# Performance work log

Measured on AMD Instinct MI355X. Metric: run time of the kernel, lower is better.

## Reference

```python
import jax, jax.numpy as jnp
import numpy as np

E = 8        # moe_num_experts
TOPK = 2     # moe_topk
H = 1024     # hidden_size
I = 1024     # intermediate_size
ISH = I * 2  # shared experts intermediate (intermediate_size * moe_num_shared_experts)
B, S = 2, 1024


def setup_inputs() -> dict:
    key = jax.random.key(0)
    ks = jax.random.split(key, 7)
    s = 0.02
    return {
        "hidden_states": jax.random.normal(ks[0], (B, S, H), jnp.float32),
        "w_router": jax.random.normal(ks[1], (H, E), jnp.float32) * s,
        "fc1_w": jax.random.normal(ks[2], (E, H, 2 * I), jnp.float32) * s,
        "fc2_w": jax.random.normal(ks[3], (E, I, H), jnp.float32) * s,
        "gate_w": jax.random.normal(ks[4], (H, ISH), jnp.float32) * s,
        "up_w": jax.random.normal(ks[5], (H, ISH), jnp.float32) * s,
        "down_w": jax.random.normal(ks[6], (ISH, H), jnp.float32) * s,
    }


def reference(hidden_states, w_router, fc1_w, fc2_w, gate_w, up_w, down_w):
    orig_shape = hidden_states.shape
    x = hidden_states.reshape(-1, orig_shape[-1])  # [N, H]

    # --- router: top-k + softmax over the top-k logits ---
    logits = x @ w_router                               # [N, E]
    top_logits, top_idx = jax.lax.top_k(logits, TOPK)   # [N, K]
    scores = jax.nn.softmax(top_logits, axis=-1)        # [N, K]

    # --- permute tokens so same-expert tokens are contiguous ---
    flat_idx = top_idx.reshape(-1)                      # [N*K]
    sorted_idx = jnp.argsort(flat_idx)                  # [N*K]
    permuted = x[sorted_idx // TOPK]                    # [N*K, H]
    eid = flat_idx[sorted_idx]                          # expert id per permuted slot

    # --- grouped expert SwiGLU MLP (masked per-expert GEMMs; masked rows
    #     contribute exactly zero since silu(0)*0 = 0 and 0 @ W = 0) ---
    out_perm = jnp.zeros((permuted.shape[0], orig_shape[-1]), x.dtype)
    for e in range(E):
        m = (eid == e).astype(x.dtype)[:, None]         # [N*K, 1]
        h1 = (permuted * m) @ fc1_w[e]                  # [N*K, 2I]
        proj, gate = jnp.split(h1, 2, axis=-1)
        out_perm = out_perm + (jax.nn.silu(proj) * gate) @ fc2_w[e]

    # --- unpermute and combine with router scores ---
    unperm = jnp.zeros_like(out_perm).at[sorted_idx].set(out_perm)  # [N*K, H]
    moe_out = (unperm.reshape(-1, TOPK, orig_shape[-1]) * scores[:, :, None]).sum(axis=1)
    moe_out = moe_out.reshape(orig_shape)

    # --- shared experts (LlamaMLP, SwiGLU) ---
    shared = (jax.nn.silu(hidden_states @ gate_w) * (hidden_states @ up_w)) @ down_w
    return moe_out + shared
```

## Files before the change

kernel.cpp:

```cpp
#include <hip/hip_runtime.h>
#include <cstdint>


#define E_ 8
#define H_ 1024
#define I_ 1024
#define ISH_ 2048
#define NTOK 2048

typedef unsigned short u16;
using bf16x8 = __attribute__((ext_vector_type(8))) __bf16;
using f32x4  = __attribute__((ext_vector_type(4))) float;

__device__ __forceinline__ u16 f2bf(float f) {
  union { float f; unsigned u; } v; v.f = f;
  unsigned r = v.u + 0x7fffu + ((v.u >> 16) & 1u);
  return (u16)(r >> 16);
}
__device__ __forceinline__ float bf2f(u16 u) {
  union { unsigned u; float f; } v; v.u = ((unsigned)u) << 16; return v.f;
}

typedef __attribute__((address_space(1))) const void glb_v;
typedef __attribute__((address_space(3))) void lds_v;
__device__ __forceinline__ void gl16(const void* g, void* l) {
  __builtin_amdgcn_global_load_lds((glb_v*)g, (lds_v*)l, 16, 0, 0);
}

__device__ __forceinline__ void router_body(const float* __restrict__ x,
                                            const float* __restrict__ wr,
                                            float* __restrict__ scores,
                                            int* __restrict__ cnt,
                                            int* __restrict__ list, int tk) {
  int lane = threadIdx.x & 63;
  const float* xr = x + (size_t)tk * H_;
  float acc[E_];
#pragma unroll
  for (int e = 0; e < E_; ++e) acc[e] = 0.f;
  int h0 = lane * 16;
#pragma unroll 4
  for (int i = 0; i < 16; ++i) {
    float xv = xr[h0 + i];
    const float* w = wr + (size_t)(h0 + i) * E_;
#pragma unroll
    for (int e = 0; e < E_; ++e) acc[e] = fmaf(xv, w[e], acc[e]);
  }
#pragma unroll
  for (int off = 32; off > 0; off >>= 1) {
#pragma unroll
    for (int e = 0; e < E_; ++e) acc[e] += __shfl_xor(acc[e], off, 64);
  }
  if (lane == 0) {
    int e0 = 0; float m0 = acc[0];
#pragma unroll
    for (int e = 1; e < E_; ++e) if (acc[e] > m0) { m0 = acc[e]; e0 = e; }
    int e1 = -1; float m1 = -1e30f;
#pragma unroll
    for (int e = 0; e < E_; ++e) if (e != e0 && acc[e] > m1) { m1 = acc[e]; e1 = e; }
    float s0 = 1.f / (1.f + __expf(m1 - m0));
    scores[tk * 2 + 0] = s0;
    scores[tk * 2 + 1] = 1.f - s0;
    int p0 = atomicAdd(&cnt[e0], 1); list[e0 * NTOK + p0] = tk * 2;
    int p1 = atomicAdd(&cnt[e1], 1); list[e1 * NTOK + p1] = tk * 2 + 1;
  }
}


__global__ __launch_bounds__(256) void prep_k(
    const float* __restrict__ x, const float* __restrict__ wr,
    float* __restrict__ scores, int* __restrict__ cnt, int* __restrict__ list,
    u16* __restrict__ xb,
    const float* __restrict__ fc1, const float* __restrict__ fc2,
    const float* __restrict__ gw, const float* __restrict__ uw,
    const float* __restrict__ dw,
    u16* __restrict__ fc1T, u16* __restrict__ fc2T, u16* __restrict__ gwT,
    u16* __restrict__ uwT, u16* __restrict__ dwT) {
  __shared__ u16 lt[64][72];
  int bid = blockIdx.x, t = threadIdx.x;
  if (bid < 512) {
    router_body(x, wr, scores, cnt, list, bid * 4 + (t >> 6));
    return;
  }
  if (bid < 1024) {
    const float4* srcx = (const float4*)x;
    ushort4* dstx = (ushort4*)xb;
    int base = (bid - 512) * 1024 + t;
#pragma unroll
    for (int it = 0; it < 4; ++it) {
      float4 v = srcx[base + it * 256];
      ushort4 o;
      o.x = f2bf(v.x); o.y = f2bf(v.y); o.z = f2bf(v.z); o.w = f2bf(v.w);
      dstx[base + it * 256] = o;
    }
    return;
  }
  int r2 = bid - 1024;
  const float* src; u16* dst; int K, N, k0, n0;
  if (r2 < 4096) {
    int e = r2 >> 9, q = r2 & 511;
    src = fc1 + ((size_t)e << 21); dst = fc1T + ((size_t)e << 21);
    K = 1024; N = 2048; k0 = (q & 15) << 6; n0 = (q >> 4) << 6;
  } else if (r2 < 6144) {
    int rr = r2 - 4096; int e = rr >> 8, q = rr & 255;
    src = fc2 + ((size_t)e << 20); dst = fc2T + ((size_t)e << 20);
    K = 1024; N = 1024; k0 = (q & 15) << 6; n0 = (q >> 4) << 6;
  } else if (r2 < 6656) {
    int q = r2 - 6144; src = gw; dst = gwT;
    K = 1024; N = 2048; k0 = (q & 15) << 6; n0 = (q >> 4) << 6;
  } else if (r2 < 7168) {
    int q = r2 - 6656; src = uw; dst = uwT;
    K = 1024; N = 2048; k0 = (q & 15) << 6; n0 = (q >> 4) << 6;
  } else {
    int q = r2 - 7168; src = dw; dst = dwT;
    K = 2048; N = 1024; k0 = (q & 31) << 6; n0 = (q >> 5) << 6;
  }
#pragma unroll
  for (int it = 0; it < 4; ++it) {
    int lin = it * 256 + t; int rr = lin >> 4, c4 = lin & 15;
    float4 v = *(const float4*)(src + (size_t)(k0 + rr) * N + n0 + c4 * 4);
    lt[c4 * 4 + 0][rr] = f2bf(v.x);
    lt[c4 * 4 + 1][rr] = f2bf(v.y);
    lt[c4 * 4 + 2][rr] = f2bf(v.z);
    lt[c4 * 4 + 3][rr] = f2bf(v.w);
  }
  __syncthreads();
#pragma unroll
  for (int it = 0; it < 2; ++it) {
    int lin = it * 256 + t; int n = lin >> 3, kq = lin & 7;
    uint4 o = *(const uint4*)&lt[n][kq * 8];
    *(uint4*)(dst + (size_t)(n0 + n) * K + k0 + kq * 8) = o;
  }
}

__global__ __launch_bounds__(256, 2) void swiglu_f_k(
    const u16* __restrict__ xb, const int* __restrict__ cnt,
    const int* __restrict__ list, const u16* __restrict__ fc1T,
    const u16* __restrict__ gwT, const u16* __restrict__ uwT,
    u16* __restrict__ act, u16* __restrict__ tmp) {
  __shared__ u16 As[128][32];
  __shared__ u16 B1s[128][32];
  __shared__ u16 B2s[128][32];
  int bid = blockIdx.x;
  int m0, n0, Me, obase = 0, ldo;
  const u16 *B1, *B2;
  const int* rowmap = nullptr;
  u16* Out;
  if (bid < 256) {
    int mb = bid >> 4, nb = bid & 15;
    m0 = mb * 128; n0 = nb * 128; Me = NTOK;
    B1 = gwT + (size_t)n0 * 1024; B2 = uwT + (size_t)n0 * 1024;
    Out = tmp; ldo = ISH_;
  } else {
    int b2 = bid - 256; int e = b2 >> 7, r = b2 & 127, mb = r >> 3, nb = r & 7;
    Me = cnt[e]; m0 = mb * 128;
    if (m0 >= Me) return;
    n0 = nb * 128;
    rowmap = list + e * NTOK;
    const u16* fe = fc1T + ((size_t)e << 21);
    B1 = fe + (size_t)n0 * 1024;
    B2 = fe + (size_t)(1024 + n0) * 1024;
    int off = 0;
    for (int q = 0; q < e; ++q) off += cnt[q];
    obase = off;
    Out = act; ldo = I_;
  }
  int t = threadIdx.x, wid = t >> 6, lane = t & 63;
  int wm = wid & 1, wn = wid >> 1, lr = lane & 15, lkg = lane >> 4;
  int cq = lane & 3, crw = lane >> 2;

  const u16 *arow[2], *b1row[2], *b2row[2];
#pragma unroll
  for (int i = 0; i < 2; ++i) {
    int c = wid * 2 + i;
    int rl = m0 + c * 16 + crw;
    int rc = rl < Me ? rl : (Me - 1);
    int tok = rowmap ? (rowmap[rc] >> 1) : rc;
    arow[i] = xb + (size_t)tok * 1024 + cq * 8;
    int rb = c * 16 + crw;
    b1row[i] = B1 + (size_t)rb * 1024 + cq * 8;
    b2row[i] = B2 + (size_t)rb * 1024 + cq * 8;
  }
  u16* aL[2]; u16* b1L[2]; u16* b2L[2];
#pragma unroll
  for (int i = 0; i < 2; ++i) {
    int c = wid * 2 + i;
    aL[i] = (u16*)As + c * 512;
    b1L[i] = (u16*)B1s + c * 512;
    b2L[i] = (u16*)B2s + c * 512;
  }

  f32x4 aP[4][4] = {}, aG[4][4] = {};
  for (int k0 = 0; k0 < 1024; k0 += 32) {
#pragma unroll
    for (int i = 0; i < 2; ++i) {
      gl16(arow[i] + k0, aL[i]);
      gl16(b1row[i] + k0, b1L[i]);
      gl16(b2row[i] + k0, b2L[i]);
    }
    __syncthreads();
    bf16x8 af[4];
#pragma unroll
    for (int f = 0; f < 4; ++f)
      af[f] = *reinterpret_cast<const bf16x8*>(&As[wm * 64 + f * 16 + lr][lkg * 8]);
#pragma unroll
    for (int fn = 0; fn < 4; ++fn) {
      bf16x8 b1 = *reinterpret_cast<const bf16x8*>(&B1s[wn * 64 + fn * 16 + lr][lkg * 8]);
      bf16x8 b2 = *reinterpret_cast<const bf16x8*>(&B2s[wn * 64 + fn * 16 + lr][lkg * 8]);
#pragma unroll
      for (int fm = 0; fm < 4; ++fm) {
        aP[fm][fn] = __builtin_amdgcn_mfma_f32_16x16x32_bf16(af[fm], b1, aP[fm][fn], 0, 0, 0);
        aG[fm][fn] = __builtin_amdgcn_mfma_f32_16x16x32_bf16(af[fm], b2, aG[fm][fn], 0, 0, 0);
      }
    }
    __syncthreads();
  }
#pragma unroll
  for (int fm = 0; fm < 4; ++fm)
#pragma unroll
    for (int fn = 0; fn < 4; ++fn)
#pragma unroll
      for (int j = 0; j < 4; ++j) {
        int row = m0 + wm * 64 + fm * 16 + lkg * 4 + j;
        if (row < Me) {
          float p = aP[fm][fn][j], g = aG[fm][fn][j];
          float s = p / (1.f + __expf(-p)) * g;
          Out[(size_t)(obase + row) * ldo + n0 + wn * 64 + fn * 16 + lr] = f2bf(s);
        }
      }
}

template <int MODE>
__global__ __launch_bounds__(256, 2) void gemm_f_k(
    const u16* __restrict__ A, const u16* __restrict__ Bg,
    const int* __restrict__ cnt, const int* __restrict__ list,
    const float* __restrict__ scores, u16* __restrict__ outb,
    const u16* __restrict__ outb_r, float* __restrict__ out) {
  constexpr int BNx = MODE == 0 ? 128 : 64;
  constexpr int FN = BNx / 32;
  constexpr int KK = MODE == 0 ? 1024 : 2048;
  constexpr int BCH = BNx / 64;
  __shared__ u16 As[128][32];
  __shared__ u16 Bs[BNx][32];
  int bid = blockIdx.x;
  int e = 0, m0, n0, Me;
  const u16 *Ab, *Bb;
  if (MODE == 0) {
    e = bid >> 7; int r = bid & 127, mb = r >> 3, nb = r & 7;
    Me = cnt[e]; m0 = mb * 128;
    if (m0 >= Me) return;
    n0 = nb * 128;
    int off = 0;
    for (int q = 0; q < e; ++q) off += cnt[q];
    Ab = A + (size_t)off * KK;
    Bb = Bg + ((size_t)e << 20) + (size_t)n0 * KK;
  } else {
    int mb = bid >> 4, nb = bid & 15;
    m0 = mb * 128; n0 = nb * 64; Me = NTOK;
    Ab = A; Bb = Bg + (size_t)n0 * KK;
  }
  int t = threadIdx.x, wid = t >> 6, lane = t & 63;
  int wm = wid & 1, wn = wid >> 1, lr = lane & 15, lkg = lane >> 4;
  int cq = lane & 3, crw = lane >> 2;

  const u16* arow[2];
#pragma unroll
  for (int i = 0; i < 2; ++i) {
    int c = wid * 2 + i;
    int rl = m0 + c * 16 + crw;
    int rc = rl < Me ? rl : (Me - 1);
    arow[i] = Ab + (size_t)rc * KK + cq * 8;
  }
  const u16* brow[BCH];
#pragma unroll
  for (int i = 0; i < BCH; ++i) {
    int c = wid * BCH + i;
    brow[i] = Bb + (size_t)(c * 16 + crw) * KK + cq * 8;
  }

  f32x4 acc[4][FN] = {};
  for (int k0 = 0; k0 < KK; k0 += 32) {
#pragma unroll
    for (int i = 0; i < 2; ++i) gl16(arow[i] + k0, (u16*)As + (wid * 2 + i) * 512);
#pragma unroll
    for (int i = 0; i < BCH; ++i) gl16(brow[i] + k0, (u16*)Bs + (wid * BCH + i) * 512);
    __syncthreads();
    bf16x8 af[4];
#pragma unroll
    for (int f = 0; f < 4; ++f)
      af[f] = *reinterpret_cast<const bf16x8*>(&As[wm * 64 + f * 16 + lr][lkg * 8]);
#pragma unroll
    for (int fn = 0; fn < FN; ++fn) {
      bf16x8 bb = *reinterpret_cast<const bf16x8*>(&Bs[wn * (BNx / 2) + fn * 16 + lr][lkg * 8]);
#pragma unroll
      for (int fm = 0; fm < 4; ++fm)
        acc[fm][fn] = __builtin_amdgcn_mfma_f32_16x16x32_bf16(af[fm], bb, acc[fm][fn], 0, 0, 0);
    }
    __syncthreads();
  }
#pragma unroll
  for (int fm = 0; fm < 4; ++fm)
#pragma unroll
    for (int fn = 0; fn < FN; ++fn)
#pragma unroll
      for (int j = 0; j < 4; ++j) {
        int row = m0 + wm * 64 + fm * 16 + lkg * 4 + j;
        if (row < Me) {
          float v = acc[fm][fn][j];
          int c = n0 + wn * (BNx / 2) + fn * 16 + lr;
          if (MODE == 0) {
            int slot = list[e * NTOK + row];
            outb[(size_t)slot * H_ + c] = f2bf(v * scores[slot]);
          } else {
            out[(size_t)row * H_ + c] =
                v + bf2f(outb_r[(size_t)(2 * row) * H_ + c]) +
                bf2f(outb_r[(size_t)(2 * row + 1) * H_ + c]);
          }
        }
      }
}

#define BM 128
#define BN 64
#define BK 32
#define PK (BK + 8)

__global__ void router_k(const float* __restrict__ x, const float* __restrict__ wr,
                         float* __restrict__ scores, int* __restrict__ cnt,
                         int* __restrict__ list) {
  int wid = threadIdx.x >> 6;
  int tk = blockIdx.x * 4 + wid;
  if (tk >= NTOK) return;
  router_body(x, wr, scores, cnt, list, tk);
}

__global__ void offs_k(const int* __restrict__ cnt, int* __restrict__ offs) {
  if (threadIdx.x == 0 && blockIdx.x == 0) {
    int s = 0;
    for (int e = 0; e < E_; ++e) { offs[e] = s; s += cnt[e]; }
  }
}

__global__ void cvt_k(const float* __restrict__ x, u16* __restrict__ xb, int n4) {
  int i = blockIdx.x * blockDim.x + threadIdx.x;
  if (i >= n4) return;
  float4 v = reinterpret_cast<const float4*>(x)[i];
  ushort4 o;
  o.x = f2bf(v.x); o.y = f2bf(v.y); o.z = f2bf(v.z); o.w = f2bf(v.w);
  reinterpret_cast<ushort4*>(xb)[i] = o;
}

template <int EXPERT>
__global__ __launch_bounds__(256) void swiglu_gemm_k(
    const u16* __restrict__ A, int lda,
    const int* __restrict__ list, const int* __restrict__ cnt, const int* __restrict__ offs,
    const float* __restrict__ B1g, const float* __restrict__ B2g, int ldb, long long bstride,
    u16* __restrict__ Out, int ldo, int K) {
  __shared__ u16 As[BM][PK];
  __shared__ u16 Bs[2][BN][PK];
  int e = EXPERT ? blockIdx.z : 0;
  int Me = EXPERT ? cnt[e] : NTOK;
  int m0 = blockIdx.y * BM;
  if (m0 >= Me) return;
  int n0 = blockIdx.x * BN;
  const int* rowmap = EXPERT ? (list + e * NTOK) : nullptr;
  const float* B1 = B1g + (EXPERT ? (long long)e * bstride : 0);
  const float* B2 = B2g + (EXPERT ? (long long)e * bstride : 0);
  int t = threadIdx.x, wid = t >> 6, lane = t & 63;
  int wm = wid & 1, wn = wid >> 1, lr = lane & 15, lkg = lane >> 4;
  f32x4 accP[4][2] = {}, accG[4][2] = {};
  for (int k0 = 0; k0 < K; k0 += BK) {
#pragma unroll
    for (int it = 0; it < 2; ++it) {
      int idx = it * 256 + t, r = idx >> 2, q = idx & 3, row = m0 + r;
      uint4 v = make_uint4(0u, 0u, 0u, 0u);
      if (row < Me) {
        int rg = EXPERT ? (rowmap[row] >> 1) : row;
        v = *reinterpret_cast<const uint4*>(A + (size_t)rg * lda + k0 + q * 8);
      }
      *reinterpret_cast<uint4*>(&As[r][q * 8]) = v;
    }
#pragma unroll
    for (int b = 0; b < 2; ++b) {
      const float* Bp = b ? B2 : B1;
#pragma unroll
      for (int it = 0; it < 2; ++it) {
        int idx = (it * 256 + t) * 4, kr = idx >> 6, c = idx & 63;
        float4 f = *reinterpret_cast<const float4*>(Bp + (size_t)(k0 + kr) * ldb + n0 + c);
        Bs[b][c + 0][kr] = f2bf(f.x); Bs[b][c + 1][kr] = f2bf(f.y);
        Bs[b][c + 2][kr] = f2bf(f.z); Bs[b][c + 3][kr] = f2bf(f.w);
      }
    }
    __syncthreads();
    bf16x8 af[4];
#pragma unroll
    for (int fm = 0; fm < 4; ++fm)
      af[fm] = *reinterpret_cast<const bf16x8*>(&As[wm * 64 + fm * 16 + lr][lkg * 8]);
#pragma unroll
    for (int fn = 0; fn < 2; ++fn) {
      bf16x8 bp = *reinterpret_cast<const bf16x8*>(&Bs[0][wn * 32 + fn * 16 + lr][lkg * 8]);
      bf16x8 bg = *reinterpret_cast<const bf16x8*>(&Bs[1][wn * 32 + fn * 16 + lr][lkg * 8]);
#pragma unroll
      for (int fm = 0; fm < 4; ++fm) {
        accP[fm][fn] = __builtin_amdgcn_mfma_f32_16x16x32_bf16(af[fm], bp, accP[fm][fn], 0, 0, 0);
        accG[fm][fn] = __builtin_amdgcn_mfma_f32_16x16x32_bf16(af[fm], bg, accG[fm][fn], 0, 0, 0);
      }
    }
    __syncthreads();
  }
#pragma unroll
  for (int fm = 0; fm < 4; ++fm)
#pragma unroll
    for (int fn = 0; fn < 2; ++fn)
#pragma unroll
      for (int j = 0; j < 4; ++j) {
        int grow = wm * 64 + fm * 16 + lkg * 4 + j, gcol = wn * 32 + fn * 16 + lr;
        int row = m0 + grow;
        if (row < Me) {
          float p = accP[fm][fn][j], g = accG[fm][fn][j];
          float s = p / (1.f + __expf(-p)) * g;
          int orow = EXPERT ? (offs[e] + row) : row;
          Out[(size_t)orow * ldo + n0 + gcol] = f2bf(s);
        }
      }
}

template <int EXPERT>
__global__ __launch_bounds__(256) void out_gemm_k(
    const u16* __restrict__ A, int lda,
    const int* __restrict__ cnt, const int* __restrict__ offs,
    const int* __restrict__ list, const float* __restrict__ scores,
    const float* __restrict__ Bg, int ldb, long long bstride,
    float* __restrict__ Out, const float* __restrict__ outbuf, int K) {
  __shared__ u16 As[BM][PK];
  __shared__ u16 Bs[BN][PK];
  int e = EXPERT ? blockIdx.z : 0;
  int Me = EXPERT ? cnt[e] : NTOK;
  int m0 = blockIdx.y * BM;
  if (m0 >= Me) return;
  int n0 = blockIdx.x * BN;
  const float* B = Bg + (EXPERT ? (long long)e * bstride : 0);
  int aoff = EXPERT ? offs[e] : 0;
  int t = threadIdx.x, wid = t >> 6, lane = t & 63;
  int wm = wid & 1, wn = wid >> 1, lr = lane & 15, lkg = lane >> 4;
  f32x4 acc[4][2] = {};
  for (int k0 = 0; k0 < K; k0 += BK) {
#pragma unroll
    for (int it = 0; it < 2; ++it) {
      int idx = it * 256 + t, r = idx >> 2, q = idx & 3, row = m0 + r;
      uint4 v = make_uint4(0u, 0u, 0u, 0u);
      if (row < Me)
        v = *reinterpret_cast<const uint4*>(A + (size_t)(aoff + row) * lda + k0 + q * 8);
      *reinterpret_cast<uint4*>(&As[r][q * 8]) = v;
    }
#pragma unroll
    for (int it = 0; it < 2; ++it) {
      int idx = (it * 256 + t) * 4, kr = idx >> 6, c = idx & 63;
      float4 f = *reinterpret_cast<const float4*>(B + (size_t)(k0 + kr) * ldb + n0 + c);
      Bs[c + 0][kr] = f2bf(f.x); Bs[c + 1][kr] = f2bf(f.y);
      Bs[c + 2][kr] = f2bf(f.z); Bs[c + 3][kr] = f2bf(f.w);
    }
    __syncthreads();
    bf16x8 af[4];
#pragma unroll
    for (int fm = 0; fm < 4; ++fm)
      af[fm] = *reinterpret_cast<const bf16x8*>(&As[wm * 64 + fm * 16 + lr][lkg * 8]);
#pragma unroll
    for (int fn = 0; fn < 2; ++fn) {
      bf16x8 bb = *reinterpret_cast<const bf16x8*>(&Bs[wn * 32 + fn * 16 + lr][lkg * 8]);
#pragma unroll
      for (int fm = 0; fm < 4; ++fm)
        acc[fm][fn] = __builtin_amdgcn_mfma_f32_16x16x32_bf16(af[fm], bb, acc[fm][fn], 0, 0, 0);
    }
    __syncthreads();
  }
#pragma unroll
  for (int fm = 0; fm < 4; ++fm)
#pragma unroll
    for (int fn = 0; fn < 2; ++fn)
#pragma unroll
      for (int j = 0; j < 4; ++j) {
        int grow = wm * 64 + fm * 16 + lkg * 4 + j, gcol = wn * 32 + fn * 16 + lr;
        int row = m0 + grow;
        if (row < Me) {
          float v = acc[fm][fn][j];
          int c = n0 + gcol;
          if (EXPERT) {
            int slot = list[e * NTOK + row];
            Out[(size_t)slot * H_ + c] = v * scores[slot];
          } else {
            Out[(size_t)row * H_ + c] =
                v + outbuf[(size_t)(2 * row) * H_ + c] + outbuf[(size_t)(2 * row + 1) * H_ + c];
          }
        }
      }
}

extern "C" void kernel_launch(void* const* d_in, const int* in_sizes, int n_in,
                              void* d_out, int out_size, void* d_ws, size_t ws_size,
                              hipStream_t stream) {
  const float* x   = (const float*)d_in[0];
  const float* wr  = (const float*)d_in[1];
  const float* fc1 = (const float*)d_in[2];
  const float* fc2 = (const float*)d_in[3];
  const float* gw  = (const float*)d_in[4];
  const float* uw  = (const float*)d_in[5];
  const float* dw  = (const float*)d_in[6];
  float* out = (float*)d_out;
  char* ws = (char*)d_ws;

  const size_t NEED_FAST = 131072ull + (88ull << 20);
  if (ws_size >= NEED_FAST) {
    float* scores = (float*)ws;
    int* cnt  = (int*)(ws + 16384);
    int* list = (int*)(ws + 16512);
    u16* xb   = (u16*)(ws + 131072);
    u16* act  = (u16*)(ws + 131072 + (4ll << 20));
    u16* tmp  = (u16*)(ws + 131072 + (12ll << 20));
    u16* outb = (u16*)(ws + 131072 + (20ll << 20));
    u16* fc1T = (u16*)(ws + 131072 + (28ll << 20));
    u16* fc2T = (u16*)(ws + 131072 + (60ll << 20));
    u16* gwT  = (u16*)(ws + 131072 + (76ll << 20));
    u16* uwT  = (u16*)(ws + 131072 + (80ll << 20));
    u16* dwT  = (u16*)(ws + 131072 + (84ll << 20));

    hipMemsetAsync(cnt, 0, 128, stream);
    prep_k<<<8704, 256, 0, stream>>>(x, wr, scores, cnt, list, xb,
                                     fc1, fc2, gw, uw, dw, fc1T, fc2T, gwT, uwT, dwT);
    swiglu_f_k<<<1280, 256, 0, stream>>>(xb, cnt, list, fc1T, gwT, uwT, act, tmp);
    gemm_f_k<0><<<1024, 256, 0, stream>>>(act, fc2T, cnt, list, scores, outb, nullptr, nullptr);
    gemm_f_k<1><<<256, 256, 0, stream>>>(tmp, dwT, nullptr, nullptr, nullptr, nullptr, outb, out);
  } else {
    float* scores = (float*)(ws);
    int*   cnt    = (int*)(ws + (16 << 10));
    int*   offs   = (int*)(ws + (16 << 10) + 128);
    int*   list   = (int*)(ws + (16 << 10) + 256);
    u16*   xb     = (u16*)(ws + (96 << 10));
    u16*   act    = (u16*)(ws + (96 << 10) + (4ll << 20));
    u16*   tmp    = (u16*)(ws + (96 << 10) + (12ll << 20));
    float* outbuf = (float*)(ws + (96 << 10) + (20ll << 20));

    hipMemsetAsync(cnt, 0, E_ * sizeof(int), stream);
    router_k<<<NTOK / 4, 256, 0, stream>>>(x, wr, scores, cnt, list);
    offs_k<<<1, 64, 0, stream>>>(cnt, offs);
    cvt_k<<<(NTOK * H_ / 4 + 255) / 256, 256, 0, stream>>>(x, xb, NTOK * H_ / 4);
    swiglu_gemm_k<1><<<dim3(I_ / BN, NTOK / BM, E_), 256, 0, stream>>>(
        xb, H_, list, cnt, offs, fc1, fc1 + I_, 2 * I_, (long long)H_ * 2 * I_, act, I_, H_);
    out_gemm_k<1><<<dim3(H_ / BN, NTOK / BM, E_), 256, 0, stream>>>(
        act, I_, cnt, offs, list, scores, fc2, H_, (long long)I_ * H_, outbuf, nullptr, I_);
    swiglu_gemm_k<0><<<dim3(ISH_ / BN, NTOK / BM, 1), 256, 0, stream>>>(
        xb, H_, nullptr, nullptr, nullptr, gw, uw, ISH_, 0, tmp, ISH_, H_);
    out_gemm_k<0><<<dim3(H_ / BN, NTOK / BM, 1), 256, 0, stream>>>(
        tmp, ISH_, nullptr, nullptr, nullptr, nullptr, dw, H_, 0, out, outbuf, ISH_);
  }
  (void)in_sizes; (void)n_in; (void)out_size;
}
```

Before: 252.6 us.

## Overlap fc2/down weight transposes with SwiGLU GEMM and split-K final GEMM

```diff
diff --git a/kernel.cpp b/kernel.cpp
--- a/kernel.cpp
+++ b/kernel.cpp
@@ -19,6 +19,9 @@
 }
 __device__ __forceinline__ float bf2f(u16 u) {
   union { unsigned u; float f; } v; v.u = ((unsigned)u) << 16; return v.f;
+}
+__device__ __forceinline__ unsigned pk2(float lo, float hi) {
+  return ((unsigned)f2bf(hi) << 16) | (unsigned)f2bf(lo);
 }
 
 typedef __attribute__((address_space(1))) const void glb_v;
@@ -65,17 +68,45 @@
   }
 }
 
+__device__ __forceinline__ void wtrans(const float* __restrict__ src,
+                                       u16* __restrict__ dst, int K, int N,
+                                       int k0, int n0, void* smem) {
+  unsigned* lt = (unsigned*)smem;
+  int t = threadIdx.x;
+  int c = t & 31, kb = t >> 5;
+  const float* sp = src + (size_t)(k0 + kb * 8) * N + n0 + (c << 2);
+  float v[8][4];
+#pragma unroll
+  for (int j2 = 0; j2 < 8; ++j2) {
+    float4 f = *(const float4*)(sp + (size_t)j2 * N);
+    v[j2][0] = f.x; v[j2][1] = f.y; v[j2][2] = f.z; v[j2][3] = f.w;
+  }
+#pragma unroll
+  for (int j = 0; j < 4; ++j) {
+    int nl = (c << 2) + j;
+    uint4 o = make_uint4(pk2(v[0][j], v[1][j]), pk2(v[2][j], v[3][j]),
+                         pk2(v[4][j], v[5][j]), pk2(v[6][j], v[7][j]));
+    *(uint4*)&lt[nl * 32 + ((kb ^ (c & 7)) << 2)] = o;
+  }
+  __syncthreads();
+#pragma unroll
+  for (int it = 0; it < 4; ++it) {
+    int lin = it * 256 + t;
+    int nl = lin >> 3, kq = lin & 7;
+    uint4 o = *(const uint4*)&lt[nl * 32 + ((kq ^ ((nl >> 2) & 7)) << 2)];
+    *(uint4*)(dst + (size_t)(n0 + nl) * K + k0 + kq * 8) = o;
+  }
+}
+
 
 __global__ __launch_bounds__(256) void prep_k(
     const float* __restrict__ x, const float* __restrict__ wr,
     float* __restrict__ scores, int* __restrict__ cnt, int* __restrict__ list,
     u16* __restrict__ xb,
-    const float* __restrict__ fc1, const float* __restrict__ fc2,
-    const float* __restrict__ gw, const float* __restrict__ uw,
-    const float* __restrict__ dw,
-    u16* __restrict__ fc1T, u16* __restrict__ fc2T, u16* __restrict__ gwT,
-    u16* __restrict__ uwT, u16* __restrict__ dwT) {
-  __shared__ u16 lt[64][72];
+    const float* __restrict__ fc1, const float* __restrict__ gw,
+    const float* __restrict__ uw,
+    u16* __restrict__ fc1T, u16* __restrict__ gwT, u16* __restrict__ uwT) {
+  __shared__ __align__(16) char psm[16384];
   int bid = blockIdx.x, t = threadIdx.x;
   if (bid < 512) {
     router_body(x, wr, scores, cnt, list, bid * 4 + (t >> 6));
@@ -94,41 +125,17 @@
     }
     return;
   }
-  int r2 = bid - 1024;
-  const float* src; u16* dst; int K, N, k0, n0;
-  if (r2 < 4096) {
-    int e = r2 >> 9, q = r2 & 511;
-    src = fc1 + ((size_t)e << 21); dst = fc1T + ((size_t)e << 21);
-    K = 1024; N = 2048; k0 = (q & 15) << 6; n0 = (q >> 4) << 6;
-  } else if (r2 < 6144) {
-    int rr = r2 - 4096; int e = rr >> 8, q = rr & 255;
-    src = fc2 + ((size_t)e << 20); dst = fc2T + ((size_t)e << 20);
-    K = 1024; N = 1024; k0 = (q & 15) << 6; n0 = (q >> 4) << 6;
-  } else if (r2 < 6656) {
-    int q = r2 - 6144; src = gw; dst = gwT;
-    K = 1024; N = 2048; k0 = (q & 15) << 6; n0 = (q >> 4) << 6;
-  } else if (r2 < 7168) {
-    int q = r2 - 6656; src = uw; dst = uwT;
-    K = 1024; N = 2048; k0 = (q & 15) << 6; n0 = (q >> 4) << 6;
+  if (bid < 3072) {
+    int b = bid - 1024;
+    int e = b >> 8, q = b & 255;
+    wtrans(fc1 + ((size_t)e << 21), fc1T + ((size_t)e << 21), 1024, 2048,
+           (q & 15) * 64, (q >> 4) * 128, psm);
+  } else if (bid < 3328) {
+    int q = bid - 3072;
+    wtrans(gw, gwT, 1024, 2048, (q & 15) * 64, (q >> 4) * 128, psm);
   } else {
-    int q = r2 - 7168; src = dw; dst = dwT;
-    K = 2048; N = 1024; k0 = (q & 31) << 6; n0 = (q >> 5) << 6;
-  }
-#pragma unroll
-  for (int it = 0; it < 4; ++it) {
-    int lin = it * 256 + t; int rr = lin >> 4, c4 = lin & 15;
-    float4 v = *(const float4*)(src + (size_t)(k0 + rr) * N + n0 + c4 * 4);
-    lt[c4 * 4 + 0][rr] = f2bf(v.x);
-    lt[c4 * 4 + 1][rr] = f2bf(v.y);
-    lt[c4 * 4 + 2][rr] = f2bf(v.z);
-    lt[c4 * 4 + 3][rr] = f2bf(v.w);
-  }
-  __syncthreads();
-#pragma unroll
-  for (int it = 0; it < 2; ++it) {
-    int lin = it * 256 + t; int n = lin >> 3, kq = lin & 7;
-    uint4 o = *(const uint4*)&lt[n][kq * 8];
-    *(uint4*)(dst + (size_t)(n0 + n) * K + k0 + kq * 8) = o;
+    int q = bid - 3328;
+    wtrans(uw, uwT, 1024, 2048, (q & 15) * 64, (q >> 4) * 128, psm);
   }
 }
 
@@ -136,11 +143,27 @@
     const u16* __restrict__ xb, const int* __restrict__ cnt,
     const int* __restrict__ list, const u16* __restrict__ fc1T,
     const u16* __restrict__ gwT, const u16* __restrict__ uwT,
-    u16* __restrict__ act, u16* __restrict__ tmp) {
-  __shared__ u16 As[128][32];
-  __shared__ u16 B1s[128][32];
-  __shared__ u16 B2s[128][32];
-  int bid = blockIdx.x;
+    u16* __restrict__ act, u16* __restrict__ tmp,
+    const float* __restrict__ fc2, const float* __restrict__ dw,
+    u16* __restrict__ fc2T, u16* __restrict__ dwT) {
+  __shared__ __align__(16) char smem[24576];
+  if (blockIdx.x & 1) {
+    int r = blockIdx.x >> 1;
+    if (r < 1024) {
+      int e = r >> 7, q = r & 127;
+      wtrans(fc2 + ((size_t)e << 20), fc2T + ((size_t)e << 20), 1024, 1024,
+             (q & 15) * 64, (q >> 4) * 128, smem);
+    } else {
+      int q = r - 1024;
+      wtrans(dw, dwT, 2048, 1024, (q & 31) * 64, (q >> 5) * 128, smem);
+    }
+    return;
+  }
+  u16 (*As)[32]  = (u16(*)[32])smem;
+  u16 (*B1s)[32] = (u16(*)[32])(smem + 8192);
+  u16 (*B2s)[32] = (u16(*)[32])(smem + 16384);
+
+  int bid = blockIdx.x >> 1;
   int m0, n0, Me, obase = 0, ldo;
   const u16 *B1, *B2;
   const int* rowmap = nullptr;
@@ -180,22 +203,15 @@
     b1row[i] = B1 + (size_t)rb * 1024 + cq * 8;
     b2row[i] = B2 + (size_t)rb * 1024 + cq * 8;
   }
-  u16* aL[2]; u16* b1L[2]; u16* b2L[2];
-#pragma unroll
-  for (int i = 0; i < 2; ++i) {
-    int c = wid * 2 + i;
-    aL[i] = (u16*)As + c * 512;
-    b1L[i] = (u16*)B1s + c * 512;
-    b2L[i] = (u16*)B2s + c * 512;
-  }
 
   f32x4 aP[4][4] = {}, aG[4][4] = {};
   for (int k0 = 0; k0 < 1024; k0 += 32) {
 #pragma unroll
     for (int i = 0; i < 2; ++i) {
-      gl16(arow[i] + k0, aL[i]);
-      gl16(b1row[i] + k0, b1L[i]);
-      gl16(b2row[i] + k0, b2L[i]);
+      int c = wid * 2 + i;
+      gl16(arow[i] + k0, (u16*)As + c * 512);
+      gl16(b1row[i] + k0, (u16*)B1s + c * 512);
+      gl16(b2row[i] + k0, (u16*)B2s + c * 512);
     }
     __syncthreads();
     bf16x8 af[4];
@@ -242,7 +258,7 @@
   __shared__ u16 As[128][32];
   __shared__ u16 Bs[BNx][32];
   int bid = blockIdx.x;
-  int e = 0, m0, n0, Me;
+  int e = 0, m0, n0, Me, ks = 0;
   const u16 *Ab, *Bb;
   if (MODE == 0) {
     e = bid >> 7; int r = bid & 127, mb = r >> 3, nb = r & 7;
@@ -254,9 +270,11 @@
     Ab = A + (size_t)off * KK;
     Bb = Bg + ((size_t)e << 20) + (size_t)n0 * KK;
   } else {
-    int mb = bid >> 4, nb = bid & 15;
+    ks = bid >> 8; int r = bid & 255;
+    int mb = r >> 4, nb = r & 15;
     m0 = mb * 128; n0 = nb * 64; Me = NTOK;
-    Ab = A; Bb = Bg + (size_t)n0 * KK;
+    Ab = A + ks * 1024;
+    Bb = Bg + (size_t)n0 * KK + ks * 1024;
   }
   int t = threadIdx.x, wid = t >> 6, lane = t & 63;
   int wm = wid & 1, wn = wid >> 1, lr = lane & 15, lkg = lane >> 4;
@@ -278,7 +296,7 @@
   }
 
   f32x4 acc[4][FN] = {};
-  for (int k0 = 0; k0 < KK; k0 += 32) {
+  for (int k0 = 0; k0 < 1024; k0 += 32) {
 #pragma unroll
     for (int i = 0; i < 2; ++i) gl16(arow[i] + k0, (u16*)As + (wid * 2 + i) * 512);
 #pragma unroll
@@ -311,9 +329,10 @@
             int slot = list[e * NTOK + row];
             outb[(size_t)slot * H_ + c] = f2bf(v * scores[slot]);
           } else {
-            out[(size_t)row * H_ + c] =
-                v + bf2f(outb_r[(size_t)(2 * row) * H_ + c]) +
-                bf2f(outb_r[(size_t)(2 * row + 1) * H_ + c]);
+            if (ks == 0)
+              v += bf2f(outb_r[(size_t)(2 * row) * H_ + c]) +
+                   bf2f(outb_r[(size_t)(2 * row + 1) * H_ + c]);
+            atomicAdd(&out[(size_t)row * H_ + c], v);
           }
         }
       }
@@ -524,11 +543,13 @@
     u16* dwT  = (u16*)(ws + 131072 + (84ll << 20));
 
     hipMemsetAsync(cnt, 0, 128, stream);
-    prep_k<<<8704, 256, 0, stream>>>(x, wr, scores, cnt, list, xb,
-                                     fc1, fc2, gw, uw, dw, fc1T, fc2T, gwT, uwT, dwT);
-    swiglu_f_k<<<1280, 256, 0, stream>>>(xb, cnt, list, fc1T, gwT, uwT, act, tmp);
+    hipMemsetAsync(out, 0, (size_t)NTOK * H_ * sizeof(float), stream);
+    prep_k<<<3584, 256, 0, stream>>>(x, wr, scores, cnt, list, xb,
+                                     fc1, gw, uw, fc1T, gwT, uwT);
+    swiglu_f_k<<<2560, 256, 0, stream>>>(xb, cnt, list, fc1T, gwT, uwT, act, tmp,
+                                         fc2, dw, fc2T, dwT);
     gemm_f_k<0><<<1024, 256, 0, stream>>>(act, fc2T, cnt, list, scores, outb, nullptr, nullptr);
-    gemm_f_k<1><<<256, 256, 0, stream>>>(tmp, dwT, nullptr, nullptr, nullptr, nullptr, outb, out);
+    gemm_f_k<1><<<512, 256, 0, stream>>>(tmp, dwT, nullptr, nullptr, nullptr, nullptr, outb, out);
   } else {
     float* scores = (float*)(ws);
     int*   cnt    = (int*)(ws + (16 << 10));
```

Result: slower. 274.4 us (+8.6%).
